# Kernel tuning notes

Measured on AMD Instinct MI355X. Metric: run time of the kernel, lower is better.

The kernel has to match this reference:

```python
import jax, jax.numpy as jnp
import numpy as np

N, D, H, E, K = 16384, 1024, 4096, 8, 2
EPS = 1e-5


def setup_inputs() -> dict:
    key = jax.random.key(0)
    ks = jax.random.split(key, 12)
    s = 0.02
    return {
        "x": jax.random.normal(ks[0], (N, D), dtype=jnp.float32),
        "ln_g": jnp.ones((D,), jnp.float32),
        "ln_b": jnp.zeros((D,), jnp.float32),
        "r_w1": jax.random.normal(ks[1], (D, H // 2), jnp.float32) * s,
        "r_b1": jnp.zeros((H // 2,), jnp.float32),
        "r_w2": jax.random.normal(ks[2], (H // 2, E), jnp.float32) * s,
        "r_b2": jnp.zeros((E,), jnp.float32),
        "e_w1": jax.random.normal(ks[3], (E, D, H), jnp.float32) * s,
        "e_b1": jnp.zeros((E, H), jnp.float32),
        "e_w2": jax.random.normal(ks[4], (E, H, D), jnp.float32) * s,
        "e_b2": jnp.zeros((E, D), jnp.float32),
    }


def reference(x, ln_g, ln_b, r_w1, r_b1, r_w2, r_b2, e_w1, e_b1, e_w2, e_b2):
    # LayerNorm
    mu = jnp.mean(x, axis=-1, keepdims=True)
    var = jnp.mean(jnp.square(x - mu), axis=-1, keepdims=True)
    xn = (x - mu) * jax.lax.rsqrt(var + EPS) * ln_g + ln_b  # [N, D]

    # Router: Linear -> ReLU -> Linear -> softmax -> top-k, renormalize
    logits = jax.nn.relu(xn @ r_w1 + r_b1) @ r_w2 + r_b2  # [N, E]
    probs = jax.nn.softmax(logits, axis=-1)
    vals, idx = jax.lax.top_k(probs, K)  # [N, K]
    vals = vals / jnp.sum(vals, axis=-1, keepdims=True)

    # Dense expert dispatch: loop over fixed small E, weight by combine gate
    out = jnp.zeros_like(x)
    for e in range(E):
        gate = jnp.sum(vals * (idx == e).astype(vals.dtype), axis=-1)  # [N]
        h = jax.nn.relu(xn @ e_w1[e] + e_b1[e])  # dropout in eval mode -> identity
        y = h @ e_w2[e] + e_b2[e]  # [N, D]
        out = out + gate[:, None] * y
    return x + out
```

## Files before the change

### kernel.cpp

```cpp
#include <hip/hip_runtime.h>
#include <cstdint>
#include <cstddef>

typedef unsigned short u16;
typedef __attribute__((ext_vector_type(8))) short bf16x8;
typedef __attribute__((ext_vector_type(4))) float f32x4;

#define N_TOK 16384
#define DIM   1024
#define HID   4096
#define NEXP  8
#define HR    2048
#define TAU   0.02f
#define MAXMT 264
#define MAXMT2 136

__device__ __forceinline__ u16 f2bf(float f) {
  union { float f; uint32_t u; } x; x.f = f;
  uint32_t r = x.u + 0x7FFFu + ((x.u >> 16) & 1u);
  return (u16)(r >> 16);
}
__device__ __forceinline__ float bf2f(u16 u) {
  union { uint32_t u; float f; } x; x.u = ((uint32_t)u) << 16; return x.f;
}

__device__ __forceinline__ void async16(const void* g, const void* l) {
  auto gp = reinterpret_cast<const __attribute__((address_space(1))) uint32_t*>(
      reinterpret_cast<uintptr_t>(g));
  auto lp = reinterpret_cast<__attribute__((address_space(3))) uint32_t*>(
      reinterpret_cast<uintptr_t>(l));
  __builtin_amdgcn_global_load_lds(gp, lp, 16, 0, 0);
}

__device__ __forceinline__ unsigned xcd_swz(unsigned flat, unsigned nwg) {
  const unsigned xcd = flat & 7u, lid = flat >> 3;
  const unsigned q = nwg >> 3, r = nwg & 7u;
  return (xcd < r ? xcd * (q + 1u) : r * (q + 1u) + (xcd - r) * q) + lid;
}

template<bool SPLIT>
__global__ __launch_bounds__(256)
void transpose_cvt(const float* __restrict__ src, u16* __restrict__ hi,
                   u16* __restrict__ lo, int R, int C)
{
  __shared__ float tile[32][33];
  const size_t bofs = (size_t)blockIdx.z * R * C;
  src += bofs; hi += bofs; if (SPLIT) lo += bofs;
  const int tx = threadIdx.x, ty = threadIdx.y;
  const int c0 = blockIdx.x * 32, r0 = blockIdx.y * 32;
#pragma unroll
  for (int i = 0; i < 4; ++i)
    tile[ty + i * 8][tx] = src[(size_t)(r0 + ty + i * 8) * C + c0 + tx];
  __syncthreads();
#pragma unroll
  for (int i = 0; i < 4; ++i) {
    float v = tile[tx][ty + i * 8];
    size_t o = (size_t)(c0 + ty + i * 8) * R + r0 + tx;
    u16 h = f2bf(v);
    hi[o] = h;
    if (SPLIT) lo[o] = f2bf(v - bf2f(h));
  }
}

__global__ __launch_bounds__(256)
void ln_kernel(const float* __restrict__ x, const float* __restrict__ g,
               const float* __restrict__ b, u16* __restrict__ xh,
               u16* __restrict__ xl, float* __restrict__ out)
{
  const int row = blockIdx.x;
  const int t = threadIdx.x;
  const float4 xv = ((const float4*)(x + (size_t)row * DIM))[t];
  float s = xv.x + xv.y + xv.z + xv.w;
  float q = xv.x * xv.x + xv.y * xv.y + xv.z * xv.z + xv.w * xv.w;
#pragma unroll
  for (int off = 32; off; off >>= 1) {
    s += __shfl_down(s, off, 64);
    q += __shfl_down(q, off, 64);
  }
  __shared__ float sm[8];
  __shared__ float mu_s, rs_s;
  const int lane = t & 63, wv = t >> 6;
  if (lane == 0) { sm[wv] = s; sm[wv + 4] = q; }
  __syncthreads();
  if (t == 0) {
    float S = sm[0] + sm[1] + sm[2] + sm[3];
    float Q = sm[4] + sm[5] + sm[6] + sm[7];
    float mu = S * (1.f / DIM);
    float var = Q * (1.f / DIM) - mu * mu;
    mu_s = mu; rs_s = rsqrtf(var + 1e-5f);
  }
  __syncthreads();
  const float mu = mu_s, rs = rs_s;
  const float4 gv = ((const float4*)g)[t];
  const float4 bv = ((const float4*)b)[t];
  float n0 = (xv.x - mu) * rs * gv.x + bv.x;
  float n1 = (xv.y - mu) * rs * gv.y + bv.y;
  float n2 = (xv.z - mu) * rs * gv.z + bv.z;
  float n3 = (xv.w - mu) * rs * gv.w + bv.w;
  ushort4 h, l;
  h.x = f2bf(n0); l.x = f2bf(n0 - bf2f(h.x));
  h.y = f2bf(n1); l.y = f2bf(n1 - bf2f(h.y));
  h.z = f2bf(n2); l.z = f2bf(n2 - bf2f(h.z));
  h.w = f2bf(n3); l.w = f2bf(n3 - bf2f(h.w));
  ((ushort4*)(xh + (size_t)row * DIM))[t] = h;
  ((ushort4*)(xl + (size_t)row * DIM))[t] = l;
  ((float4*)(out + (size_t)row * DIM))[t] = xv;
}

__global__ __launch_bounds__(256)
void logits_kernel(const u16* __restrict__ HrB, const float* __restrict__ w2,
                   float* __restrict__ logits)
{
  const int row = blockIdx.x, t = threadIdx.x;
  const u16* h = HrB + (size_t)row * HR;
  const ushort4* hv = (const ushort4*)(h + t * 8);
  ushort4 h0 = hv[0], h1 = hv[1];
  u16 hh[8] = {h0.x, h0.y, h0.z, h0.w, h1.x, h1.y, h1.z, h1.w};
  float p[8] = {0, 0, 0, 0, 0, 0, 0, 0};
#pragma unroll
  for (int j = 0; j < 8; ++j) {
    const int col = t * 8 + j;
    const float v = bf2f(hh[j]);
    const float4* wp = (const float4*)(w2 + (size_t)col * 8);
    float4 a = wp[0], b = wp[1];
    p[0] += v * a.x; p[1] += v * a.y; p[2] += v * a.z; p[3] += v * a.w;
    p[4] += v * b.x; p[5] += v * b.y; p[6] += v * b.z; p[7] += v * b.w;
  }
#pragma unroll
  for (int off = 32; off; off >>= 1)
#pragma unroll
    for (int e = 0; e < 8; ++e) p[e] += __shfl_down(p[e], off, 64);
  __shared__ float sm[4][8];
  const int lane = t & 63, wv = t >> 6;
  if (lane == 0) {
#pragma unroll
    for (int e = 0; e < 8; ++e) sm[wv][e] = p[e];
  }
  __syncthreads();
  if (t < 8)
    logits[(size_t)row * 8 + t] = sm[0][t] + sm[1][t] + sm[2][t] + sm[3][t];
}

__device__ __forceinline__ void load_logits(const float* logits, const float* b2,
                                            int row, float l[8]) {
  const float4* lp = (const float4*)(logits + (size_t)row * 8);
  float4 a = lp[0], b = lp[1];
  l[0] = a.x + b2[0]; l[1] = a.y + b2[1]; l[2] = a.z + b2[2]; l[3] = a.w + b2[3];
  l[4] = b.x + b2[4]; l[5] = b.y + b2[5]; l[6] = b.z + b2[6]; l[7] = b.w + b2[7];
}
__device__ __forceinline__ void top2(const float l[8], int& i0, float& l0,
                                     int& i1, float& l1) {
  i0 = 0; l0 = l[0];
#pragma unroll
  for (int e = 1; e < 8; ++e) if (l[e] > l0) { l0 = l[e]; i0 = e; }
  i1 = -1; l1 = -1e30f;
#pragma unroll
  for (int e = 0; e < 8; ++e) if (e != i0 && l[e] > l1) { l1 = l[e]; i1 = e; }
}

__global__ __launch_bounds__(256)
void pass_flag(float* __restrict__ logits, const float* __restrict__ b2,
               int* __restrict__ fixL, int* __restrict__ cntFix)
{
  __shared__ int lcnt;
  __shared__ int base;
  const int t = threadIdx.x;
  const int row = blockIdx.x * 256 + t;
  if (t == 0) lcnt = 0;
  float l[8]; load_logits(logits, b2, row, l);
  int i0, i1; float l0, l1;
  top2(l, i0, l0, i1, l1);
  float l2 = -1e30f;
#pragma unroll
  for (int e = 0; e < 8; ++e)
    if (e != i0 && e != i1 && l[e] > l2) l2 = l[e];
  const bool flag = (l1 - l2) < TAU;
  __syncthreads();
  int r = 0;
  if (flag) r = atomicAdd(&lcnt, 1);
  __syncthreads();
  if (t == 0) base = atomicAdd(cntFix, lcnt);
  __syncthreads();
  if (flag) {
    fixL[base + r] = row;
    float4 z = {0.f, 0.f, 0.f, 0.f};
    ((float4*)(logits + (size_t)row * 8))[0] = z;
    ((float4*)(logits + (size_t)row * 8))[1] = z;
  }
}

__global__ __launch_bounds__(256)
void pass_count(const float* __restrict__ logits, const float* __restrict__ b2,
                int* __restrict__ cnts)
{
  __shared__ int lcnt[NEXP];
  const int t = threadIdx.x;
  const int row = blockIdx.x * 256 + t;
  if (t < NEXP) lcnt[t] = 0;
  float l[8]; load_logits(logits, b2, row, l);
  int i0, i1; float l0, l1;
  top2(l, i0, l0, i1, l1);
  __syncthreads();
  atomicAdd(&lcnt[i0], 1);
  atomicAdd(&lcnt[i1], 1);
  __syncthreads();
  if (t < NEXP) atomicAdd(&cnts[t], lcnt[t]);
}

__global__ void scan_kernel(const int* __restrict__ cnts, int* __restrict__ offs,
                            int* __restrict__ tileOffs, int* __restrict__ tileOffs2)
{
  if (threadIdx.x == 0) {
    int s = 0, ts = 0, ts2 = 0;
#pragma unroll
    for (int e = 0; e < NEXP; ++e) {
      offs[e] = s; s += cnts[e];
      tileOffs[e] = ts; ts += (cnts[e] + 127) >> 7;
      tileOffs2[e] = ts2; ts2 += (cnts[e] + 255) >> 8;
    }
    offs[NEXP] = s;
    tileOffs[NEXP] = ts;
    tileOffs2[NEXP] = ts2;
  }
}

__global__ __launch_bounds__(256)
void pass_scatter(const float* __restrict__ logits, const float* __restrict__ b2,
                  const int* __restrict__ offs, int* __restrict__ cnts2,
                  int* __restrict__ rowsC, float* __restrict__ gateC)
{
  __shared__ int lcnt[NEXP];
  __shared__ int sbase[NEXP];
  const int t = threadIdx.x;
  const int row = blockIdx.x * 256 + t;
  if (t < NEXP) lcnt[t] = 0;
  float l[8]; load_logits(logits, b2, row, l);
  int i0, i1; float l0, l1;
  top2(l, i0, l0, i1, l1);
  float tt = expf(l1 - l0);
  float g0 = 1.f / (1.f + tt);
  float g1 = tt / (1.f + tt);
  __syncthreads();
  int r0 = atomicAdd(&lcnt[i0], 1);
  int r1 = atomicAdd(&lcnt[i1], 1);
  __syncthreads();
  if (t < NEXP) sbase[t] = atomicAdd(&cnts2[t], lcnt[t]);
  __syncthreads();
  int p0 = offs[i0] + sbase[i0] + r0;
  int p1 = offs[i1] + sbase[i1] + r1;
  rowsC[p0] = row; gateC[p0] = g0;
  rowsC[p1] = row; gateC[p1] = g1;
}

#define G8_BAR() do { __builtin_amdgcn_s_barrier(); \
                      __builtin_amdgcn_sched_barrier(0); } while (0)
#define G8_VM4() asm volatile("s_waitcnt vmcnt(4)" ::: "memory")
#define G8_VM0() asm volatile("s_waitcnt vmcnt(0)" ::: "memory")

#define READ_A(aL, mfh, Af) do { \
  _Pragma("unroll") for (int mf = 0; mf < 4; ++mf) { \
    Af[mf][0] = *(const bf16x8*)&(aL)[((mfh)*4+mf)*1024 + aBase + swzC[0]]; \
    Af[mf][1] = *(const bf16x8*)&(aL)[((mfh)*4+mf)*1024 + aBase + swzC[1]]; \
  } } while (0)

#define READ_B(bL, nfh, Bf) do { \
  _Pragma("unroll") for (int nf = 0; nf < 2; ++nf) { \
    Bf[nf][0] = *(const bf16x8*)&(bL)[((nfh)*2+nf)*1024 + bBase + swzC[0]]; \
    Bf[nf][1] = *(const bf16x8*)&(bL)[((nfh)*2+nf)*1024 + bBase + swzC[1]]; \
  } } while (0)

#define MFMA_Q(mfh, nfh, Af, Bf) do { \
  __builtin_amdgcn_s_setprio(1); \
  _Pragma("unroll") for (int mf = 0; mf < 4; ++mf) \
  _Pragma("unroll") for (int nf = 0; nf < 2; ++nf) { \
    acc[(mfh)*4+mf][(nfh)*2+nf] = __builtin_amdgcn_mfma_f32_16x16x32_bf16( \
        Af[mf][0], Bf[nf][0], acc[(mfh)*4+mf][(nfh)*2+nf], 0, 0, 0); \
    acc[(mfh)*4+mf][(nfh)*2+nf] = __builtin_amdgcn_mfma_f32_16x16x32_bf16( \
        Af[mf][1], Bf[nf][1], acc[(mfh)*4+mf][(nfh)*2+nf], 0, 0, 0); \
  } \
  __builtin_amdgcn_s_setprio(0); } while (0)

template<int EPI, bool GATHER, bool DENSE>
__global__ __launch_bounds__(512, 2)
void gemm8p(const u16* __restrict__ A0, const u16* __restrict__ B0,
            int lda, int ldb, int K, int NT, int Mdense,
            size_t bStrideE, int biasStrideE,
            const int* __restrict__ counts, const int* __restrict__ offs,
            const int* __restrict__ tileOffs,
            const int* __restrict__ rowsC, const float* __restrict__ gatesC,
            const float* __restrict__ bias,
            u16* __restrict__ Cbf, float* __restrict__ Cf32, int ldc)
{
  const unsigned swz = xcd_swz(blockIdx.x, gridDim.x);
  const int mt = (int)(swz / (unsigned)NT);
  int e, m0, Mq, off;
  if constexpr (DENSE) {
    if (mt >= Mdense / 256) return;
    e = 0; m0 = mt * 256; Mq = Mdense; off = 0;
  } else {
    if (mt >= tileOffs[NEXP]) return;
    e = 0;
#pragma unroll
    for (int i = 1; i < NEXP; ++i) if (tileOffs[i] <= mt) e = i;
    m0 = (mt - tileOffs[e]) * 256;
    Mq = counts[e];
    if (m0 >= Mq) return;
    off = offs[e];
  }
  const int n0 = (int)(swz % (unsigned)NT) * 256;
  const int* rows = DENSE ? nullptr : (rowsC + off);
  const u16* B = B0 + (size_t)e * bStrideE;
  const float* bi = bias + (size_t)e * biasStrideE;

  __shared__ alignas(16) u16 As[2][2][128 * 64];
  __shared__ alignas(16) u16 Bs[2][2][128 * 64];

  const int t = threadIdx.x;
  const int numK = K >> 6;

  const u16* aP[2][2]; const u16* bP[2][2]; int dst[2];
#pragma unroll
  for (int j = 0; j < 2; ++j) {
    const int gdx = j * 512 + t;
    const int rw = gdx >> 3;
    const int cs = ((gdx & 7) ^ (rw & 7)) << 3;
    dst[j] = gdx * 8;
#pragma unroll
    for (int h = 0; h < 2; ++h) {
      const int grow = m0 + h * 128 + rw;
      if constexpr (DENSE) {
        aP[h][j] = A0 + (size_t)grow * lda + cs;
      } else {
        const int amc = grow < Mq ? grow : (Mq - 1);
        const size_t agr = GATHER ? (size_t)rows[amc] : (size_t)(off + amc);
        aP[h][j] = A0 + agr * lda + cs;
      }
      bP[h][j] = B + (size_t)(n0 + h * 128 + rw) * ldb + cs;
    }
  }

  auto stA = [&](int tile, int h) {
    async16(aP[h][0] + (size_t)tile * 64, &As[tile & 1][h][dst[0]]);
    async16(aP[h][1] + (size_t)tile * 64, &As[tile & 1][h][dst[1]]);
  };
  auto stB = [&](int tile, int h) {
    async16(bP[h][0] + (size_t)tile * 64, &Bs[tile & 1][h][dst[0]]);
    async16(bP[h][1] + (size_t)tile * 64, &Bs[tile & 1][h][dst[1]]);
  };

  const int lane = t & 63, wv = t >> 6;
  const int wr = wv >> 2;
  const int wc = wv & 3;
  const int fr = lane & 15, fq = lane >> 4;

  int swzC[2];
#pragma unroll
  for (int ks = 0; ks < 2; ++ks)
    swzC[ks] = ((ks * 4 + fq) ^ (fr & 7)) << 3;
  const int aBase = fr * 64;
  const int bBase = (wc & 1) * 4096 + fr * 64;

  const u16* aH[2] = { &As[0][wr][0], &As[1][wr][0] };
  const u16* bH[2] = { &Bs[0][wc >> 1][0], &Bs[1][wc >> 1][0] };

  f32x4 acc[8][4];
#pragma unroll
  for (int i = 0; i < 8; ++i)
#pragma unroll
    for (int j = 0; j < 4; ++j) acc[i][j] = (f32x4){0.f, 0.f, 0.f, 0.f};

  stB(0, 0); stB(0, 1); stA(0, 0); stA(0, 1);
  stB(1, 0); stB(1, 1);
  G8_VM4();
  G8_BAR();

  bf16x8 Af[4][2], Bf0[2][2], Bf1[2][2];

  const int numI = numK >> 1;
  for (int it = 0; it < numI; ++it) {
    const int t1 = 2 * it + 1, t2 = 2 * it + 2, t3 = 2 * it + 3;
    const bool last = (t2 >= numK);
    READ_A(aH[0], 0, Af);
    READ_B(bH[0], 0, Bf0);
    stA(t1, 0);
    G8_BAR();
    MFMA_Q(0, 0, Af, Bf0);
    G8_BAR();
    READ_B(bH[0], 1, Bf1);
    stA(t1, 1);
    G8_BAR();
    MFMA_Q(0, 1, Af, Bf1);
    G8_BAR();
    READ_A(aH[0], 1, Af);
    if (!last) stB(t2, 0);
    G8_BAR();
    MFMA_Q(1, 1, Af, Bf1);
    G8_BAR();
    if (!last) stB(t2, 1);
    G8_BAR();
    MFMA_Q(1, 0, Af, Bf0);
    if (last) { G8_VM0(); } else { G8_VM4(); }
    G8_BAR();
    READ_A(aH[1], 0, Af);
    READ_B(bH[1], 0, Bf0);
    if (!last) stA(t2, 0);
    G8_BAR();
    MFMA_Q(0, 0, Af, Bf0);
    G8_BAR();
    READ_B(bH[1], 1, Bf1);
    if (!last) stA(t2, 1);
    G8_BAR();
    MFMA_Q(0, 1, Af, Bf1);
    G8_BAR();
    READ_A(aH[1], 1, Af);
    if (t3 < numK) stB(t3, 0);
    G8_BAR();
    MFMA_Q(1, 1, Af, Bf1);
    G8_BAR();
    if (t3 < numK) stB(t3, 1);
    G8_BAR();
    MFMA_Q(1, 0, Af, Bf0);
    if (!last) { G8_VM4(); }
    G8_BAR();
  }

  float bv[4];
#pragma unroll
  for (int nf = 0; nf < 4; ++nf) bv[nf] = bi[n0 + wc * 64 + nf * 16 + fr];

  const int crowBase = DENSE ? 0 : off;
#pragma unroll
  for (int mf = 0; mf < 8; ++mf)
#pragma unroll
    for (int r = 0; r < 4; ++r) {
      const int m = m0 + wr * 128 + mf * 16 + fq * 4 + r;
      if (m < Mq) {
        if constexpr (EPI == 2) {
          const size_t orow = (size_t)rows[m];
          const float g = gatesC[off + m];
#pragma unroll
          for (int nf = 0; nf < 4; ++nf) {
            const int n = n0 + wc * 64 + nf * 16 + fr;
            atomicAdd(&Cf32[orow * ldc + n], g * (acc[mf][nf][r] + bv[nf]));
          }
        } else {
#pragma unroll
          for (int nf = 0; nf < 4; ++nf) {
            const int n = n0 + wc * 64 + nf * 16 + fr;
            Cbf[(size_t)(crowBase + m) * ldc + n] =
                f2bf(fmaxf(acc[mf][nf][r] + bv[nf], 0.f));
          }
        }
      }
    }
}

template<bool SPLIT, int EPI, bool GATHER>
__global__ __launch_bounds__(256, 2)
void gemm_bt(const u16* __restrict__ A0, const u16* __restrict__ A1,
             const u16* __restrict__ B0, const u16* __restrict__ B1,
             int lda, int ldb, int K, int M,
             const int* __restrict__ counts, int expertArg,
             const int* __restrict__ offs,
             const int* __restrict__ rowsC, const float* __restrict__ gatesC,
             const float* __restrict__ bias,
             const float* __restrict__ w2, float* __restrict__ logits,
             u16* __restrict__ Cbf, float* __restrict__ Cf32, int ldc)
{
  int expert, m0, n0;
  if (counts == nullptr) {
    const unsigned nwg = gridDim.x * gridDim.y;
    const unsigned flat = blockIdx.y * gridDim.x + blockIdx.x;
    const unsigned swz = xcd_swz(flat, nwg);
    expert = expertArg;
    m0 = (int)(swz / gridDim.x) * 128;
    n0 = (int)(swz % gridDim.x) * 128;
  } else {
    expert = expertArg;
    m0 = blockIdx.y * 128;
    n0 = blockIdx.x * 128;
  }

  const int Mq = counts ? counts[expert] : M;
  if (m0 >= Mq) return;
  const int off = offs ? offs[expert] : 0;
  const int* rows = rowsC ? rowsC + off : nullptr;
  const float* gates = gatesC ? gatesC + off : nullptr;
  const u16* B = B0;
  const u16* Bl = SPLIT ? B1 : nullptr;
  const float* bi = bias;
  const int z = (int)blockIdx.z;
  const int zOff = z * K;

  __shared__ u16 As0[128 * 32], Bs0[128 * 32];
  __shared__ u16 As1[SPLIT ? 128 * 32 : 8], Bs1[SPLIT ? 128 * 32 : 8];

  const int t = threadIdx.x;
  size_t aoff[2]; int acodd[2]; size_t boff[2];
#pragma unroll
  for (int i = 0; i < 2; ++i) {
    int gdx = i * 256 + t;
    int ar = gdx >> 2, ac = (gdx & 3) * 8;
    int am = m0 + ar;
    int amc = am < Mq ? am : (Mq - 1);
    int agr = GATHER ? rows[amc] : amc;
    aoff[i] = (size_t)agr * lda + ac + zOff;
    boff[i] = (size_t)(n0 + ar) * ldb + ac + zOff;
    acodd[i] = gdx * 8;
  }

  f32x4 acc[4][4];
#pragma unroll
  for (int i = 0; i < 4; ++i)
#pragma unroll
    for (int j = 0; j < 4; ++j) acc[i][j] = (f32x4){0.f, 0.f, 0.f, 0.f};

  const int lane = t & 63, wv = t >> 6;
  const int wm = (wv >> 1) * 64, wn = (wv & 1) * 64;
  const int fr = lane & 15, fq = lane >> 4;

  for (int k0 = 0; k0 < K; k0 += 32) {
    __syncthreads();
#pragma unroll
    for (int i = 0; i < 2; ++i) {
      async16(A0 + aoff[i] + k0, &As0[acodd[i]]);
      async16(B + boff[i] + k0, &Bs0[acodd[i]]);
      if (SPLIT) {
        async16(A1 + aoff[i] + k0, &As1[acodd[i]]);
        async16(Bl + boff[i] + k0, &Bs1[acodd[i]]);
      }
    }
    __syncthreads();
    bf16x8 af[4], bfr[4], af1[4], bf1[4];
#pragma unroll
    for (int xi = 0; xi < 4; ++xi) {
      af[xi]  = *(const bf16x8*)&As0[(wm + xi * 16 + fr) * 32 + fq * 8];
      bfr[xi] = *(const bf16x8*)&Bs0[(wn + xi * 16 + fr) * 32 + fq * 8];
      if (SPLIT) {
        af1[xi] = *(const bf16x8*)&As1[(wm + xi * 16 + fr) * 32 + fq * 8];
        bf1[xi] = *(const bf16x8*)&Bs1[(wn + xi * 16 + fr) * 32 + fq * 8];
      }
    }
#pragma unroll
    for (int mt = 0; mt < 4; ++mt)
#pragma unroll
      for (int nt = 0; nt < 4; ++nt) {
        acc[mt][nt] = __builtin_amdgcn_mfma_f32_16x16x32_bf16(af[mt], bfr[nt], acc[mt][nt], 0, 0, 0);
        if (SPLIT) {
          acc[mt][nt] = __builtin_amdgcn_mfma_f32_16x16x32_bf16(af[mt], bf1[nt], acc[mt][nt], 0, 0, 0);
          acc[mt][nt] = __builtin_amdgcn_mfma_f32_16x16x32_bf16(af1[mt], bfr[nt], acc[mt][nt], 0, 0, 0);
        }
      }
  }

  if constexpr (EPI == 3) {
    float w2v[4][8]; float b1v[4];
#pragma unroll
    for (int nt = 0; nt < 4; ++nt) {
      const int n = n0 + wn + nt * 16 + fr;
      b1v[nt] = bi[n];
      const float4* wp = (const float4*)(w2 + (size_t)n * 8);
      float4 wa = wp[0], wb = wp[1];
      w2v[nt][0] = wa.x; w2v[nt][1] = wa.y; w2v[nt][2] = wa.z; w2v[nt][3] = wa.w;
      w2v[nt][4] = wb.x; w2v[nt][5] = wb.y; w2v[nt][6] = wb.z; w2v[nt][7] = wb.w;
    }
#pragma unroll
    for (int mt = 0; mt < 4; ++mt) {
      float pe[4][8];
#pragma unroll
      for (int r = 0; r < 4; ++r)
#pragma unroll
        for (int ee = 0; ee < 8; ++ee) pe[r][ee] = 0.f;
#pragma unroll
      for (int nt = 0; nt < 4; ++nt)
#pragma unroll
        for (int r = 0; r < 4; ++r) {
          float v = fmaxf(acc[mt][nt][r] + b1v[nt], 0.f);
#pragma unroll
          for (int ee = 0; ee < 8; ++ee) pe[r][ee] += v * w2v[nt][ee];
        }
#pragma unroll
      for (int offx = 1; offx < 16; offx <<= 1)
#pragma unroll
        for (int r = 0; r < 4; ++r)
#pragma unroll
          for (int ee = 0; ee < 8; ++ee)
            pe[r][ee] += __shfl_xor(pe[r][ee], offx, 64);
      if (fr == 0) {
#pragma unroll
        for (int r = 0; r < 4; ++r) {
          const int m = m0 + wm + mt * 16 + fq * 4 + r;
          if (m < Mq) {
            const int lrow = GATHER ? rows[m] : m;
#pragma unroll
            for (int ee = 0; ee < 8; ++ee)
              atomicAdd(&logits[(size_t)lrow * 8 + ee], pe[r][ee]);
          }
        }
      }
    }
    return;
  }

#pragma unroll
  for (int mt = 0; mt < 4; ++mt) {
#pragma unroll
    for (int nt = 0; nt < 4; ++nt) {
      const int n = n0 + wn + nt * 16 + fr;
      const float bvv = (z == 0) ? bi[n] : 0.f;
#pragma unroll
      for (int r = 0; r < 4; ++r) {
        const int m = m0 + wm + mt * 16 + fq * 4 + r;
        if (m < Mq) {
          float v = acc[mt][nt][r] + bvv;
          if constexpr (EPI == 1) {
            Cbf[(size_t)m * ldc + n] = f2bf(fmaxf(v, 0.f));
          } else {
            atomicAdd(&Cf32[(size_t)rows[m] * ldc + n], gates[m] * v);
          }
        }
      }
    }
  }
}

extern "C" void kernel_launch(void* const* d_in, const int* in_sizes, int n_in,
                              void* d_out, int out_size, void* d_ws, size_t ws_size,
                              hipStream_t stream)
{
  const float* x    = (const float*)d_in[0];
  const float* ln_g = (const float*)d_in[1];
  const float* ln_b = (const float*)d_in[2];
  const float* r_w1 = (const float*)d_in[3];
  const float* r_b1 = (const float*)d_in[4];
  const float* r_w2 = (const float*)d_in[5];
  const float* r_b2 = (const float*)d_in[6];
  const float* e_w1 = (const float*)d_in[7];
  const float* e_b1 = (const float*)d_in[8];
  const float* e_w2 = (const float*)d_in[9];
  const float* e_b2 = (const float*)d_in[10];
  float* out = (float*)d_out;

  char* ws = (char*)d_ws;
  const size_t MB = 1024ull * 1024ull;
  u16*   xnhi = (u16*)(ws);
  u16*   xnlo = (u16*)(ws + 32 * MB);
  u16*   rw1h = (u16*)(ws + 64 * MB);
  u16*   rw1l = (u16*)(ws + 68 * MB);
  u16*   ew1t = (u16*)(ws + 72 * MB);
  u16*   ew2t = (u16*)(ws + 136 * MB);
  float* logits = (float*)(ws + 200 * MB);
  int*   rowsC  = (int*)(ws + 200 * MB + 512 * 1024);
  float* gateC  = (float*)(ws + 200 * MB + 640 * 1024);
  int*   fixL   = (int*)(ws + 200 * MB + 768 * 1024);
  int*   cntb   = (int*)(ws + 200 * MB + 832 * 1024);
  int*   cnts   = cntb;
  int*   cnts2  = cntb + 8;
  int*   offs   = cntb + 16;
  int*   cntFix = cntb + 25;
  int*   tileOffs  = cntb + 32;
  int*   tileOffs2 = cntb + 48;
  u16*   Hbuf = (u16*)(ws + 201 * MB);
  u16*   HrB  = Hbuf;
  (void)in_sizes; (void)n_in; (void)out_size;

  const bool fused = ws_size >= 458ull * MB;

  hipMemsetAsync(cntb, 0, 256, stream);

  dim3 tb(32, 8);
  transpose_cvt<true ><<<dim3(HR / 32, DIM / 32, 1), tb, 0, stream>>>(r_w1, rw1h, rw1l, DIM, HR);
  transpose_cvt<false><<<dim3(HID / 32, DIM / 32, NEXP), tb, 0, stream>>>(e_w1, ew1t, nullptr, DIM, HID);
  transpose_cvt<false><<<dim3(DIM / 32, HID / 32, NEXP), tb, 0, stream>>>(e_w2, ew2t, nullptr, HID, DIM);

  ln_kernel<<<N_TOK, 256, 0, stream>>>(x, ln_g, ln_b, xnhi, xnlo, out);

  gemm8p<1, false, true><<<dim3((HR / 256) * (N_TOK / 256)), 512, 0, stream>>>(
      xnhi, rw1h, DIM, DIM, DIM, HR / 256, N_TOK, 0, 0,
      nullptr, nullptr, nullptr, nullptr, nullptr, r_b1,
      HrB, nullptr, HR);

  logits_kernel<<<N_TOK, 256, 0, stream>>>(HrB, r_w2, logits);

  pass_flag<<<N_TOK / 256, 256, 0, stream>>>(logits, r_b2, fixL, cntFix);

  gemm_bt<true, 3, true><<<dim3(HR / 128, N_TOK / 128), 256, 0, stream>>>(
      xnhi, xnlo, rw1h, rw1l, DIM, DIM, DIM, N_TOK,
      cntFix, 0, nullptr, fixL, nullptr, r_b1, r_w2, logits,
      nullptr, nullptr, 0);

  pass_count<<<N_TOK / 256, 256, 0, stream>>>(logits, r_b2, cnts);
  scan_kernel<<<1, 64, 0, stream>>>(cnts, offs, tileOffs, tileOffs2);
  pass_scatter<<<N_TOK / 256, 256, 0, stream>>>(logits, r_b2, offs, cnts2, rowsC, gateC);

  if (fused) {
    gemm8p<1, true, false><<<dim3((HID / 256) * MAXMT2), 512, 0, stream>>>(
        xnhi, ew1t, DIM, DIM, DIM, HID / 256, 0,
        (size_t)HID * DIM, HID,
        cnts, offs, tileOffs2, rowsC, nullptr, e_b1,
        Hbuf, nullptr, HID);
    gemm8p<2, false, false><<<dim3((DIM / 256) * MAXMT2), 512, 0, stream>>>(
        Hbuf, ew2t, HID, HID, HID, DIM / 256, 0,
        (size_t)DIM * HID, DIM,
        cnts, offs, tileOffs2, rowsC, gateC, e_b2,
        nullptr, out, DIM);
  } else {
    for (int e = 0; e < NEXP; ++e) {
      gemm_bt<false, 1, true><<<dim3(HID / 128, N_TOK / 128), 256, 0, stream>>>(
          xnhi, nullptr, ew1t + (size_t)e * HID * DIM, nullptr,
          DIM, DIM, DIM, N_TOK,
          cnts, e, offs, rowsC, nullptr, e_b1 + (size_t)e * HID, nullptr, nullptr,
          Hbuf, nullptr, HID);
      gemm_bt<false, 2, false><<<dim3(DIM / 128, N_TOK / 128, 2), 256, 0, stream>>>(
          Hbuf, nullptr, ew2t + (size_t)e * DIM * HID, nullptr,
          HID, HID, HID / 2, N_TOK,
          cnts, e, offs, rowsC, gateC, e_b2 + (size_t)e * DIM, nullptr, nullptr,
          nullptr, out, DIM);
    }
  }
}
```

Before: 1.363 ms.

## Split-K the expert down-projection GEMM and add explicit LDS waitcnts

Adds a ksplit parameter to the 256x256 MFMA GEMM and launches the second expert GEMM (K=4096, N=1024) with a K split of 2. This doubles the number of blocks, giving a grid that otherwise had only 4 N-tiles more parallelism; partial sums accumulate through the existing atomicAdd epilogue, with bias added only by the first split. It also inserts explicit lgkmcnt waits around the LDS fragment reads and reorders the MFMA loop so the k-halves are issued in sequence. The cost is twice as many fp32 atomic adds to the output.

```diff
diff --git a/kernel.cpp b/kernel.cpp
--- a/kernel.cpp
+++ b/kernel.cpp
@@ -256,6 +256,9 @@
                       __builtin_amdgcn_sched_barrier(0); } while (0)
 #define G8_VM4() asm volatile("s_waitcnt vmcnt(4)" ::: "memory")
 #define G8_VM0() asm volatile("s_waitcnt vmcnt(0)" ::: "memory")
+#define G8_LGKM0() do { asm volatile("s_waitcnt lgkmcnt(0)" ::: "memory"); \
+                        __builtin_amdgcn_sched_barrier(0); } while (0)
+#define G8_LGKM8() asm volatile("s_waitcnt lgkmcnt(8)" ::: "memory")
 
 #define READ_A(aL, mfh, Af) do { \
   _Pragma("unroll") for (int mf = 0; mf < 4; ++mf) { \
@@ -271,19 +274,17 @@
 
 #define MFMA_Q(mfh, nfh, Af, Bf) do { \
   __builtin_amdgcn_s_setprio(1); \
+  _Pragma("unroll") for (int kk = 0; kk < 2; ++kk) \
   _Pragma("unroll") for (int mf = 0; mf < 4; ++mf) \
-  _Pragma("unroll") for (int nf = 0; nf < 2; ++nf) { \
+  _Pragma("unroll") for (int nf = 0; nf < 2; ++nf) \
     acc[(mfh)*4+mf][(nfh)*2+nf] = __builtin_amdgcn_mfma_f32_16x16x32_bf16( \
-        Af[mf][0], Bf[nf][0], acc[(mfh)*4+mf][(nfh)*2+nf], 0, 0, 0); \
-    acc[(mfh)*4+mf][(nfh)*2+nf] = __builtin_amdgcn_mfma_f32_16x16x32_bf16( \
-        Af[mf][1], Bf[nf][1], acc[(mfh)*4+mf][(nfh)*2+nf], 0, 0, 0); \
-  } \
+        Af[mf][kk], Bf[nf][kk], acc[(mfh)*4+mf][(nfh)*2+nf], 0, 0, 0); \
   __builtin_amdgcn_s_setprio(0); } while (0)
 
 template<int EPI, bool GATHER, bool DENSE>
 __global__ __launch_bounds__(512, 2)
 void gemm8p(const u16* __restrict__ A0, const u16* __restrict__ B0,
-            int lda, int ldb, int K, int NT, int Mdense,
+            int lda, int ldb, int K, int NT, int ksplit, int Mdense,
             size_t bStrideE, int biasStrideE,
             const int* __restrict__ counts, const int* __restrict__ offs,
             const int* __restrict__ tileOffs,
@@ -292,7 +293,8 @@
             u16* __restrict__ Cbf, float* __restrict__ Cf32, int ldc)
 {
   const unsigned swz = xcd_swz(blockIdx.x, gridDim.x);
-  const int mt = (int)(swz / (unsigned)NT);
+  const unsigned ntks = (unsigned)(NT * ksplit);
+  const int mt = (int)(swz / ntks);
   int e, m0, Mq, off;
   if constexpr (DENSE) {
     if (mt >= Mdense / 256) return;
@@ -307,7 +309,11 @@
     if (m0 >= Mq) return;
     off = offs[e];
   }
-  const int n0 = (int)(swz % (unsigned)NT) * 256;
+  const unsigned rest = swz % ntks;
+  const int n0 = (int)(rest / (unsigned)ksplit) * 256;
+  const int ks = (int)(rest % (unsigned)ksplit);
+  const int Keff = K / ksplit;
+  const int kBase = ks * Keff;
   const int* rows = DENSE ? nullptr : (rowsC + off);
   const u16* B = B0 + (size_t)e * bStrideE;
   const float* bi = bias + (size_t)e * biasStrideE;
@@ -316,14 +322,14 @@
   __shared__ alignas(16) u16 Bs[2][2][128 * 64];
 
   const int t = threadIdx.x;
-  const int numK = K >> 6;
+  const int numK = Keff >> 6;
 
   const u16* aP[2][2]; const u16* bP[2][2]; int dst[2];
 #pragma unroll
   for (int j = 0; j < 2; ++j) {
     const int gdx = j * 512 + t;
     const int rw = gdx >> 3;
-    const int cs = ((gdx & 7) ^ (rw & 7)) << 3;
+    const int cs = (((gdx & 7) ^ (rw & 7)) << 3) + kBase;
     dst[j] = gdx * 8;
 #pragma unroll
     for (int h = 0; h < 2; ++h) {
@@ -355,8 +361,8 @@
 
   int swzC[2];
 #pragma unroll
-  for (int ks = 0; ks < 2; ++ks)
-    swzC[ks] = ((ks * 4 + fq) ^ (fr & 7)) << 3;
+  for (int kk = 0; kk < 2; ++kk)
+    swzC[kk] = ((kk * 4 + fq) ^ (fr & 7)) << 3;
   const int aBase = fr * 64;
   const int bBase = (wc & 1) * 4096 + fr * 64;
 
@@ -383,17 +389,21 @@
     READ_A(aH[0], 0, Af);
     READ_B(bH[0], 0, Bf0);
     stA(t1, 0);
-    G8_BAR();
+    G8_LGKM8();
+    G8_BAR();
+    G8_LGKM0();
     MFMA_Q(0, 0, Af, Bf0);
     G8_BAR();
     READ_B(bH[0], 1, Bf1);
     stA(t1, 1);
     G8_BAR();
+    G8_LGKM0();
     MFMA_Q(0, 1, Af, Bf1);
     G8_BAR();
     READ_A(aH[0], 1, Af);
     if (!last) stB(t2, 0);
     G8_BAR();
+    G8_LGKM0();
     MFMA_Q(1, 1, Af, Bf1);
     G8_BAR();
     if (!last) stB(t2, 1);
@@ -404,17 +414,21 @@
     READ_A(aH[1], 0, Af);
     READ_B(bH[1], 0, Bf0);
     if (!last) stA(t2, 0);
-    G8_BAR();
+    G8_LGKM8();
+    G8_BAR();
+    G8_LGKM0();
     MFMA_Q(0, 0, Af, Bf0);
     G8_BAR();
     READ_B(bH[1], 1, Bf1);
     if (!last) stA(t2, 1);
     G8_BAR();
+    G8_LGKM0();
     MFMA_Q(0, 1, Af, Bf1);
     G8_BAR();
     READ_A(aH[1], 1, Af);
     if (t3 < numK) stB(t3, 0);
     G8_BAR();
+    G8_LGKM0();
     MFMA_Q(1, 1, Af, Bf1);
     G8_BAR();
     if (t3 < numK) stB(t3, 1);
@@ -426,7 +440,10 @@
 
   float bv[4];
 #pragma unroll
-  for (int nf = 0; nf < 4; ++nf) bv[nf] = bi[n0 + wc * 64 + nf * 16 + fr];
+  for (int nf = 0; nf < 4; ++nf) {
+    bv[nf] = bi[n0 + wc * 64 + nf * 16 + fr];
+    if (EPI == 2 && ks != 0) bv[nf] = 0.f;
+  }
 
   const int crowBase = DENSE ? 0 : off;
 #pragma unroll
@@ -676,7 +693,7 @@
   ln_kernel<<<N_TOK, 256, 0, stream>>>(x, ln_g, ln_b, xnhi, xnlo, out);
 
   gemm8p<1, false, true><<<dim3((HR / 256) * (N_TOK / 256)), 512, 0, stream>>>(
-      xnhi, rw1h, DIM, DIM, DIM, HR / 256, N_TOK, 0, 0,
+      xnhi, rw1h, DIM, DIM, DIM, HR / 256, 1, N_TOK, 0, 0,
       nullptr, nullptr, nullptr, nullptr, nullptr, r_b1,
       HrB, nullptr, HR);
 
@@ -695,12 +712,12 @@
 
   if (fused) {
     gemm8p<1, true, false><<<dim3((HID / 256) * MAXMT2), 512, 0, stream>>>(
-        xnhi, ew1t, DIM, DIM, DIM, HID / 256, 0,
+        xnhi, ew1t, DIM, DIM, DIM, HID / 256, 1, 0,
         (size_t)HID * DIM, HID,
         cnts, offs, tileOffs2, rowsC, nullptr, e_b1,
         Hbuf, nullptr, HID);
-    gemm8p<2, false, false><<<dim3((DIM / 256) * MAXMT2), 512, 0, stream>>>(
-        Hbuf, ew2t, HID, HID, HID, DIM / 256, 0,
+    gemm8p<2, false, false><<<dim3((DIM / 256) * MAXMT2 * 2), 512, 0, stream>>>(
+        Hbuf, ew2t, HID, HID, HID, DIM / 256, 2, 0,
         (size_t)DIM * HID, DIM,
         cnts, offs, tileOffs2, rowsC, gateC, e_b2,
         nullptr, out, DIM);
```

Result: slower. 1.441 ms (+5.7%).
